# Optimization experiments

Hardware: AMD Instinct MI355X
Metric: run time of the kernel (lower is better)

## Reference

```python
import jax, jax.numpy as jnp
import numpy as np

B, S, D, H = 4, 2048, 256, 8
SPARSITY = 0.1


def setup_inputs() -> dict:
    key = jax.random.key(0)
    ks = jax.random.split(key, 6)
    s = 0.02
    return {
        "x": jax.random.normal(ks[0], (B, S, D), jnp.float32),
        # nn.MultiheadAttention packed in-projection (W_q;W_k;W_v) and out-projection
        "w_in": jax.random.normal(ks[1], (3 * D, D), jnp.float32) * s,
        "b_in": jnp.zeros((3 * D,), jnp.float32),
        "w_out": jax.random.normal(ks[2], (D, D), jnp.float32) * s,
        "b_out": jnp.zeros((D,), jnp.float32),
        # sparsity gate: Linear(D, D//4) -> ReLU -> Linear(D//4, 1) -> Sigmoid
        "gate_w1": jax.random.normal(ks[3], (D // 4, D), jnp.float32) * s,
        "gate_b1": jnp.zeros((D // 4,), jnp.float32),
        "gate_w2": jax.random.normal(ks[4], (1, D // 4), jnp.float32) * s,
        "gate_b2": jnp.zeros((1,), jnp.float32),
    }


def reference(x, w_in, b_in, w_out, b_out, gate_w1, gate_b1, gate_w2, gate_b2):
    b, s, d = x.shape
    hd = d // H

    # --- adaptive sparse mask (top-k importance gating) ---
    h = jax.nn.relu(jnp.einsum('bsd,fd->bsf', x, gate_w1) + gate_b1)
    importance = jax.nn.sigmoid(jnp.einsum('bsf,of->bso', h, gate_w2) + gate_b2)[..., 0]  # [B,S]
    k = max(1, int(s * SPARSITY))
    _, top_idx = jax.lax.top_k(importance, k)  # [B,k]
    keep = jnp.zeros((b, s), dtype=bool).at[jnp.arange(b)[:, None], top_idx].set(True)  # [B,S]

    # --- multi-head attention with key_padding_mask = ~keep ---
    qkv = jnp.einsum('bsd,ed->bse', x, w_in) + b_in  # [B,S,3D]
    q, kk, v = jnp.split(qkv, 3, axis=-1)
    split_heads = lambda t: t.reshape(b, s, H, hd).transpose(0, 2, 1, 3)  # [B,H,S,hd]
    q, kk, v = split_heads(q), split_heads(kk), split_heads(v)

    scores = jnp.einsum('bhqd,bhkd->bhqk', q, kk) / jnp.sqrt(jnp.asarray(hd, x.dtype))
    neg = jnp.finfo(scores.dtype).min
    scores = jnp.where(keep[:, None, None, :], scores, neg)  # mask non-selected keys
    attn = jax.nn.softmax(scores, axis=-1)

    out = jnp.einsum('bhqk,bhkd->bhqd', attn, v)
    out = out.transpose(0, 2, 1, 3).reshape(b, s, d)
    return jnp.einsum('bsd,od->bso', out, w_out) + b_out
```

## Files before the change

### kernel.cpp

```cpp
#include <hip/hip_runtime.h>
#include <hip/hip_bf16.h>

#define B_  4
#define S_  2048
#define D_  256
#define H_  8
#define HD_ 32
#define K_  204
#define SCALE_ 0.17677669529663687f

#define OFF_IMP    0
#define OFF_META   8192
#define OFF_KIDX   8208
#define OFF_KG     9232
#define OFF_VT     113680
#define OFF_Q      228368
#define OFF_XH     1276944
#define OFF_XL     2325520
#define OFF_AOH    3374096
#define OFF_AOL    4422672
#define OFF_WIH    5471248
#define OFF_WIL    5569552
#define OFF_WOH    5667856
#define OFF_WOL    5700624

#define GSTR 80
#define PSTR 228
#define VSTR 232

typedef __attribute__((ext_vector_type(8))) short short8v;
typedef __attribute__((ext_vector_type(4))) float f32x4;

static __device__ __forceinline__ unsigned short f2bf(float f) {
    unsigned int u = __float_as_uint(f);
    u += 0x7FFFu + ((u >> 16) & 1u);
    return (unsigned short)(u >> 16);
}
static __device__ __forceinline__ float bf2f(unsigned short h) {
    return __uint_as_float((unsigned int)h << 16);
}
static __device__ __forceinline__ short8v ld_bf8(const unsigned short* p) {
    union { unsigned int u[4]; short8v v; } cv;
    const uint2 a  = *(const uint2*)(p);
    const uint2 b2 = *(const uint2*)(p + 4);
    cv.u[0] = a.x; cv.u[1] = a.y; cv.u[2] = b2.x; cv.u[3] = b2.y;
    return cv.v;
}
static __device__ __forceinline__ void split_store8(
    const float* __restrict__ src, unsigned short* dh, unsigned short* dl)
{
    short8v h, l;
    #pragma unroll
    for (int e = 0; e < 8; ++e) {
        const float f = src[e];
        const unsigned short hh = f2bf(f);
        h[e] = (short)hh;
        l[e] = (short)f2bf(f - bf2f(hh));
    }
    *(short8v*)dh = h;
    *(short8v*)dl = l;
}

__global__ __launch_bounds__(256) void gate_kernel(
    const float* __restrict__ x, const float* __restrict__ gw1,
    const float* __restrict__ gb1, const float* __restrict__ gw2,
    const float* __restrict__ w_in, const float* __restrict__ w_out, float* ws)
{
    const int t0 = blockIdx.x * 8;
    const int tid = threadIdx.x;
    __shared__ __align__(16) float xs[8 * D_];
    __shared__ float hred[8 * 64];

    const float4* src = (const float4*)(x + (size_t)t0 * D_);
    ((float4*)xs)[tid]       = src[tid];
    ((float4*)xs)[tid + 256] = src[tid + 256];
    __syncthreads();

    {
        unsigned short* XH = (unsigned short*)(ws + OFF_XH);
        unsigned short* XL = (unsigned short*)(ws + OFF_XL);
        split_store8(xs + tid * 8, XH + (size_t)t0 * D_ + tid * 8,
                                   XL + (size_t)t0 * D_ + tid * 8);
    }
    if (blockIdx.x < 128) {
        const int e0 = blockIdx.x * 2048 + tid * 8;
        if (e0 < 196608) {
            split_store8(w_in + e0, (unsigned short*)(ws + OFF_WIH) + e0,
                                    (unsigned short*)(ws + OFF_WIL) + e0);
        } else {
            const int e = e0 - 196608;
            split_store8(w_out + e, (unsigned short*)(ws + OFF_WOH) + e,
                                    (unsigned short*)(ws + OFF_WOL) + e);
        }
    }
    if (blockIdx.x == 0 && tid < 16) ((int*)(ws + OFF_META))[tid] = 0;

    const int c = tid & 3, f = tid >> 2;
    float4 wv[16];
    const float4* wr = (const float4*)(gw1 + (size_t)f * D_) + c;
    #pragma unroll
    for (int j = 0; j < 16; ++j) wv[j] = wr[j * 4];
    const float bb = gb1[f], g2 = gw2[f];

    #pragma unroll
    for (int tk = 0; tk < 8; ++tk) {
        const float4* xr = (const float4*)(xs + tk * D_) + c;
        float a = 0.0f;
        #pragma unroll
        for (int j = 0; j < 16; ++j) {
            float4 xv = xr[j * 4];
            a += wv[j].x*xv.x + wv[j].y*xv.y + wv[j].z*xv.z + wv[j].w*xv.w;
        }
        a += __shfl_xor(a, 1);
        a += __shfl_xor(a, 2);
        if (c == 0) hred[tk * 64 + f] = fmaxf(a + bb, 0.0f) * g2;
    }
    __syncthreads();

    const int tk = tid >> 5, ln = tid & 31;
    float s = hred[tk * 64 + ln] + hred[tk * 64 + ln + 32];
    #pragma unroll
    for (int o = 16; o; o >>= 1) s += __shfl_xor(s, o, 32);
    if (ln == 0) ws[OFF_IMP + t0 + tk] = s;
}

__global__ __launch_bounds__(256) void rank_kernel(
    const float* __restrict__ ws_imp, int* kidx, int* meta)
{
    const int b  = blockIdx.x >> 7;
    const int ic = blockIdx.x & 127;
    const int tid = threadIdx.x;
    __shared__ __align__(16) float vs[S_];
    const float* src = ws_imp + b * S_;
    #pragma unroll
    for (int cc = 0; cc < 2; ++cc)
        ((float4*)vs)[tid + cc*256] = ((const float4*)src)[tid + cc*256];
    __syncthreads();

    const int il = tid >> 4;
    const int c  = tid & 15;
    const int i  = ic * 16 + il;
    const float vi = vs[i];
    int gt = 0, eq = 0;
    const float4* v4 = (const float4*)vs + c * 32;
    #pragma unroll 8
    for (int t = 0; t < 32; ++t) {
        const int j4 = (t + c) & 31;
        float4 w = v4[j4];
        const int base = c * 128 + j4 * 4;
        gt += (w.x > vi); eq += (w.x == vi) && (base + 0 < i);
        gt += (w.y > vi); eq += (w.y == vi) && (base + 1 < i);
        gt += (w.z > vi); eq += (w.z == vi) && (base + 2 < i);
        gt += (w.w > vi); eq += (w.w == vi) && (base + 3 < i);
    }
    int r = gt + eq;
    r += __shfl_xor(r, 1);
    r += __shfl_xor(r, 2);
    r += __shfl_xor(r, 4);
    r += __shfl_xor(r, 8);
    if (c == 0 && r < K_) {
        const int p = atomicAdd(&meta[2 + b], 1);
        kidx[b * K_ + p] = i;
    }
}

__global__ __launch_bounds__(256) void proj_kernel(
    const unsigned short* __restrict__ XH, const unsigned short* __restrict__ XL,
    const unsigned short* __restrict__ WIH, const unsigned short* __restrict__ WIL,
    const float* __restrict__ b_in, unsigned short* __restrict__ Qb,
    unsigned short* __restrict__ KG, unsigned short* __restrict__ VTg,
    const int* __restrict__ kidx)
{
    __shared__ __align__(16) unsigned short Ash[64 * GSTR];
    __shared__ __align__(16) unsigned short Asl[64 * GSTR];
    __shared__ __align__(16) unsigned short Bsh[64 * GSTR];
    __shared__ __align__(16) unsigned short Bsl[64 * GSTR];

    const int tid = threadIdx.x;
    const bool isQ = (blockIdx.x < 128);
    const int lane = tid & 63, w = tid >> 6;
    const int c = lane & 15, g = lane >> 4;
    const int mq = w >> 1, nq = w & 1;
    const int srow = tid >> 2, sseg = tid & 3;

    int m0, n0, b = blockIdx.y;
    size_t arow;
    int brow;
    if (isQ) {
        m0 = blockIdx.x * 64; n0 = blockIdx.y * 64;
        arow = (size_t)(m0 + srow);
        brow = n0 + srow;
    } else {
        const int kx = blockIdx.x - 128;
        m0 = (kx & 3) * 64; n0 = (kx >> 2) * 64;
        const int tok = kidx[b * K_ + min(m0 + srow, K_ - 1)];
        arow = (size_t)b * S_ + tok;
        brow = D_ + n0 + srow;
    }
    const unsigned short* Aph = XH + arow * D_ + sseg * 16;
    const unsigned short* Apl = XL + arow * D_ + sseg * 16;
    const unsigned short* Bph = WIH + (size_t)brow * D_ + sseg * 16;
    const unsigned short* Bpl = WIL + (size_t)brow * D_ + sseg * 16;

    const f32x4 zf = {0.0f, 0.0f, 0.0f, 0.0f};
    f32x4 acc[2][2] = {{zf, zf}, {zf, zf}};

    short8v arh[2], arl[2], brh[2], brl[2];
    #pragma unroll
    for (int u = 0; u < 2; ++u) {
        arh[u] = *(const short8v*)(Aph + u*8); arl[u] = *(const short8v*)(Apl + u*8);
        brh[u] = *(const short8v*)(Bph + u*8); brl[u] = *(const short8v*)(Bpl + u*8);
    }

    for (int k0 = 0; k0 < D_; k0 += 64) {
        __syncthreads();
        #pragma unroll
        for (int u = 0; u < 2; ++u) {
            *(short8v*)&Ash[srow*GSTR + sseg*16 + u*8] = arh[u];
            *(short8v*)&Asl[srow*GSTR + sseg*16 + u*8] = arl[u];
            *(short8v*)&Bsh[srow*GSTR + sseg*16 + u*8] = brh[u];
            *(short8v*)&Bsl[srow*GSTR + sseg*16 + u*8] = brl[u];
        }
        __syncthreads();
        if (k0 + 64 < D_) {
            #pragma unroll
            for (int u = 0; u < 2; ++u) {
                arh[u] = *(const short8v*)(Aph + k0 + 64 + u*8);
                arl[u] = *(const short8v*)(Apl + k0 + 64 + u*8);
                brh[u] = *(const short8v*)(Bph + k0 + 64 + u*8);
                brl[u] = *(const short8v*)(Bpl + k0 + 64 + u*8);
            }
        }
        #pragma unroll
        for (int ks = 0; ks < 2; ++ks) {
            short8v am[2][2], bm[2][2];
            #pragma unroll
            for (int t = 0; t < 2; ++t) {
                const int ra = (mq*32 + t*16 + c) * GSTR + ks*32 + g*8;
                am[t][0] = *(const short8v*)&Ash[ra];
                am[t][1] = *(const short8v*)&Asl[ra];
                const int rb = (nq*32 + t*16 + c) * GSTR + ks*32 + g*8;
                bm[t][0] = *(const short8v*)&Bsh[rb];
                bm[t][1] = *(const short8v*)&Bsl[rb];
            }
            #pragma unroll
            for (int mt = 0; mt < 2; ++mt)
                #pragma unroll
                for (int nt = 0; nt < 2; ++nt) {
                    acc[mt][nt] = __builtin_amdgcn_mfma_f32_16x16x32_bf16(am[mt][0], bm[nt][0], acc[mt][nt], 0, 0, 0);
                    acc[mt][nt] = __builtin_amdgcn_mfma_f32_16x16x32_bf16(am[mt][0], bm[nt][1], acc[mt][nt], 0, 0, 0);
                    acc[mt][nt] = __builtin_amdgcn_mfma_f32_16x16x32_bf16(am[mt][1], bm[nt][0], acc[mt][nt], 0, 0, 0);
                }
        }
    }

    if (isQ) {
        #pragma unroll
        for (int nt = 0; nt < 2; ++nt) {
            const int n = n0 + nq*32 + nt*16 + c;
            const float bv = b_in[n];
            #pragma unroll
            for (int mt = 0; mt < 2; ++mt) {
                const int m = m0 + mq*32 + mt*16 + g*4;
                #pragma unroll
                for (int r = 0; r < 4; ++r)
                    Qb[(size_t)(m + r) * D_ + n] = f2bf(acc[mt][nt][r] + bv);
            }
        }
    } else {
        #pragma unroll
        for (int nt = 0; nt < 2; ++nt) {
            const int n = n0 + nq*32 + nt*16 + c;
            const float bv = b_in[D_ + n];
            #pragma unroll
            for (int mt = 0; mt < 2; ++mt) {
                const int j = m0 + mq*32 + mt*16 + g*4;
                #pragma unroll
                for (int r = 0; r < 4; ++r) {
                    const int jj = j + r;
                    if (n < 256) {
                        if (jj < K_)
                            KG[((size_t)b * K_ + jj) * 256 + n] = f2bf(acc[mt][nt][r] + bv);
                    } else {
                        if (jj < 224)
                            VTg[((size_t)b * 256 + (n - 256)) * 224 + jj] =
                                (jj < K_) ? f2bf(acc[mt][nt][r] + bv) : (unsigned short)0;
                    }
                }
            }
        }
    }
}

__global__ __launch_bounds__(256) void gemm_kernel(
    const unsigned short* __restrict__ Ah, const unsigned short* __restrict__ Al,
    const unsigned short* __restrict__ Bh, const unsigned short* __restrict__ Bl,
    const float* __restrict__ bias, float* __restrict__ Cf)
{
    __shared__ __align__(16) unsigned short Ash[64 * GSTR];
    __shared__ __align__(16) unsigned short Asl[64 * GSTR];
    __shared__ __align__(16) unsigned short Bsh[64 * GSTR];
    __shared__ __align__(16) unsigned short Bsl[64 * GSTR];

    const int tid = threadIdx.x;
    const int m0 = blockIdx.x * 64, n0 = blockIdx.y * 64;
    const int lane = tid & 63, w = tid >> 6;
    const int c = lane & 15, g = lane >> 4;
    const int mq = w >> 1, nq = w & 1;

    const f32x4 zf = {0.0f, 0.0f, 0.0f, 0.0f};
    f32x4 acc[2][2] = {{zf, zf}, {zf, zf}};

    const int srow = tid >> 2, sseg = tid & 3;
    const unsigned short* Aph = Ah + (size_t)(m0 + srow) * D_ + sseg * 16;
    const unsigned short* Apl = Al + (size_t)(m0 + srow) * D_ + sseg * 16;
    const unsigned short* Bph = Bh + (size_t)(n0 + srow) * D_ + sseg * 16;
    const unsigned short* Bpl = Bl + (size_t)(n0 + srow) * D_ + sseg * 16;

    short8v arh[2], arl[2], brh[2], brl[2];
    #pragma unroll
    for (int u = 0; u < 2; ++u) {
        arh[u] = *(const short8v*)(Aph + u*8); arl[u] = *(const short8v*)(Apl + u*8);
        brh[u] = *(const short8v*)(Bph + u*8); brl[u] = *(const short8v*)(Bpl + u*8);
    }

    for (int k0 = 0; k0 < D_; k0 += 64) {
        __syncthreads();
        #pragma unroll
        for (int u = 0; u < 2; ++u) {
            *(short8v*)&Ash[srow*GSTR + sseg*16 + u*8] = arh[u];
            *(short8v*)&Asl[srow*GSTR + sseg*16 + u*8] = arl[u];
            *(short8v*)&Bsh[srow*GSTR + sseg*16 + u*8] = brh[u];
            *(short8v*)&Bsl[srow*GSTR + sseg*16 + u*8] = brl[u];
        }
        __syncthreads();
        if (k0 + 64 < D_) {
            #pragma unroll
            for (int u = 0; u < 2; ++u) {
                arh[u] = *(const short8v*)(Aph + k0 + 64 + u*8);
                arl[u] = *(const short8v*)(Apl + k0 + 64 + u*8);
                brh[u] = *(const short8v*)(Bph + k0 + 64 + u*8);
                brl[u] = *(const short8v*)(Bpl + k0 + 64 + u*8);
            }
        }
        #pragma unroll
        for (int ks = 0; ks < 2; ++ks) {
            short8v am[2][2], bm[2][2];
            #pragma unroll
            for (int t = 0; t < 2; ++t) {
                const int ra = (mq*32 + t*16 + c) * GSTR + ks*32 + g*8;
                am[t][0] = *(const short8v*)&Ash[ra];
                am[t][1] = *(const short8v*)&Asl[ra];
                const int rb = (nq*32 + t*16 + c) * GSTR + ks*32 + g*8;
                bm[t][0] = *(const short8v*)&Bsh[rb];
                bm[t][1] = *(const short8v*)&Bsl[rb];
            }
            #pragma unroll
            for (int mt = 0; mt < 2; ++mt)
                #pragma unroll
                for (int nt = 0; nt < 2; ++nt) {
                    acc[mt][nt] = __builtin_amdgcn_mfma_f32_16x16x32_bf16(am[mt][0], bm[nt][0], acc[mt][nt], 0, 0, 0);
                    acc[mt][nt] = __builtin_amdgcn_mfma_f32_16x16x32_bf16(am[mt][0], bm[nt][1], acc[mt][nt], 0, 0, 0);
                    acc[mt][nt] = __builtin_amdgcn_mfma_f32_16x16x32_bf16(am[mt][1], bm[nt][0], acc[mt][nt], 0, 0, 0);
                }
        }
    }
    #pragma unroll
    for (int nt = 0; nt < 2; ++nt) {
        const int n = n0 + nq*32 + nt*16 + c;
        const float bv = bias[n];
        #pragma unroll
        for (int mt = 0; mt < 2; ++mt) {
            const int m = m0 + mq*32 + mt*16 + g*4;
            #pragma unroll
            for (int r = 0; r < 4; ++r)
                Cf[(size_t)(m + r) * D_ + n] = acc[mt][nt][r] + bv;
        }
    }
}

__global__ __launch_bounds__(256) void attn_kernel(
    const unsigned short* __restrict__ KG, const unsigned short* __restrict__ VTg,
    const unsigned short* __restrict__ Qb,
    unsigned short* __restrict__ aoh, unsigned short* __restrict__ aol)
{
    const int b = blockIdx.z, h = blockIdx.y, q0 = blockIdx.x * 32;
    const int tid = threadIdx.x;
    const int lane = tid & 63, w = tid >> 6;
    const int c = lane & 15, g = lane >> 4;

    __shared__ __align__(16) unsigned short Pl[32 * PSTR];
    __shared__ __align__(16) unsigned short VTl[32 * VSTR];
    __shared__ float redl[4 * 32];
    __shared__ float invl[32];

    const unsigned short* KGb = KG + (size_t)b * K_ * 256;

    {
        const unsigned short* vsrc = VTg + ((size_t)b * 256 + h * HD_) * 224;
        for (int i = tid; i < 32 * 28; i += 256) {
            const int d = i / 28, seg = i % 28;
            *(short8v*)&VTl[d * VSTR + seg * 8] = *(const short8v*)(vsrc + d * 224 + seg * 8);
        }
    }
    {
        const int q = tid >> 3, cc = tid & 7;
        *(unsigned int*)&Pl[q * PSTR + 208 + cc * 2] = 0u;
    }

    short8v qa[2];
    #pragma unroll
    for (int qt = 0; qt < 2; ++qt)
        qa[qt] = *(const short8v*)(Qb + (size_t)(b * S_ + q0 + qt*16 + c) * D_ + h * HD_ + g * 8);

    const int njt = (w == 0) ? 4 : 3;
    f32x4 acc[2][4];
    const f32x4 zf = {0.0f, 0.0f, 0.0f, 0.0f};
    #pragma unroll
    for (int qt = 0; qt < 2; ++qt)
        #pragma unroll
        for (int t = 0; t < 4; ++t) acc[qt][t] = zf;

    for (int t = 0; t < njt; ++t) {
        const int jt = w + 4 * t;
        const int jc = min(jt * 16 + c, K_ - 1);
        const short8v kb = *(const short8v*)(KGb + (size_t)jc * 256 + h * HD_ + g * 8);
        acc[0][t] = __builtin_amdgcn_mfma_f32_16x16x32_bf16(qa[0], kb, acc[0][t], 0, 0, 0);
        acc[1][t] = __builtin_amdgcn_mfma_f32_16x16x32_bf16(qa[1], kb, acc[1][t], 0, 0, 0);
    }

    float rs[2][4] = {{0,0,0,0},{0,0,0,0}};
    for (int t = 0; t < njt; ++t) {
        const int jg = (w + 4 * t) * 16 + c;
        const bool val = (jg < K_);
        #pragma unroll
        for (int qt = 0; qt < 2; ++qt) {
            #pragma unroll
            for (int r = 0; r < 4; ++r) {
                const float e = val ? __expf(acc[qt][t][r] * SCALE_) : 0.0f;
                rs[qt][r] += e;
                Pl[(qt*16 + g*4 + r) * PSTR + jg] = f2bf(e);
            }
        }
    }
    #pragma unroll
    for (int qt = 0; qt < 2; ++qt)
        #pragma unroll
        for (int r = 0; r < 4; ++r) {
            float s = rs[qt][r];
            s += __shfl_xor(s, 1); s += __shfl_xor(s, 2);
            s += __shfl_xor(s, 4); s += __shfl_xor(s, 8);
            if (c == 0) redl[w * 32 + qt*16 + g*4 + r] = s;
        }

    __syncthreads();
    if (tid < 32)
        invl[tid] = 1.0f / (redl[tid] + redl[32 + tid] + redl[64 + tid] + redl[96 + tid]);
    __syncthreads();

    const int dt = w >> 1, qt2 = w & 1;
    f32x4 o = zf;
    const unsigned short* vb = &VTl[(dt*16 + c) * VSTR];
    const unsigned short* pb = &Pl[(qt2*16 + c) * PSTR];
    #pragma unroll
    for (int kt = 0; kt < 7; ++kt) {
        const short8v av = ld_bf8(vb + kt*32 + g*8);
        const short8v bv = ld_bf8(pb + kt*32 + g*8);
        o = __builtin_amdgcn_mfma_f32_16x16x32_bf16(av, bv, o, 0, 0, 0);
    }
    const float iv = invl[qt2*16 + c];
    const size_t oidx = (size_t)(b * S_ + q0 + qt2*16 + c) * D_ + h * HD_ + dt*16 + g*4;
    ushort4 hh, ll;
    {
        const float v0 = o[0]*iv, v1 = o[1]*iv, v2 = o[2]*iv, v3 = o[3]*iv;
        hh.x = f2bf(v0); ll.x = f2bf(v0 - bf2f(hh.x));
        hh.y = f2bf(v1); ll.y = f2bf(v1 - bf2f(hh.y));
        hh.z = f2bf(v2); ll.z = f2bf(v2 - bf2f(hh.z));
        hh.w = f2bf(v3); ll.w = f2bf(v3 - bf2f(hh.w));
    }
    *(ushort4*)(aoh + oidx) = hh;
    *(ushort4*)(aol + oidx) = ll;
}

extern "C" void kernel_launch(void* const* d_in, const int* in_sizes, int n_in,
                              void* d_out, int out_size, void* d_ws, size_t ws_size,
                              hipStream_t stream)
{
    const float* x     = (const float*)d_in[0];
    const float* w_in  = (const float*)d_in[1];
    const float* b_in  = (const float*)d_in[2];
    const float* w_out = (const float*)d_in[3];
    const float* b_out = (const float*)d_in[4];
    const float* gw1   = (const float*)d_in[5];
    const float* gb1   = (const float*)d_in[6];
    const float* gw2   = (const float*)d_in[7];

    float* ws = (float*)d_ws;
    int* meta = (int*)(ws + OFF_META);
    int* kidx = (int*)(ws + OFF_KIDX);
    unsigned short* KG  = (unsigned short*)(ws + OFF_KG);
    unsigned short* VTg = (unsigned short*)(ws + OFF_VT);
    unsigned short* Qb  = (unsigned short*)(ws + OFF_Q);
    unsigned short* XH  = (unsigned short*)(ws + OFF_XH);
    unsigned short* XL  = (unsigned short*)(ws + OFF_XL);
    unsigned short* AOH = (unsigned short*)(ws + OFF_AOH);
    unsigned short* AOL = (unsigned short*)(ws + OFF_AOL);
    unsigned short* WIH = (unsigned short*)(ws + OFF_WIH);
    unsigned short* WIL = (unsigned short*)(ws + OFF_WIL);
    unsigned short* WOH = (unsigned short*)(ws + OFF_WOH);
    unsigned short* WOL = (unsigned short*)(ws + OFF_WOL);
    float* out = (float*)d_out;

    gate_kernel<<<B_ * S_ / 8, 256, 0, stream>>>(x, gw1, gb1, gw2, w_in, w_out, ws);
    rank_kernel<<<B_ * 128, 256, 0, stream>>>(ws + OFF_IMP, kidx, meta);
    proj_kernel<<<dim3(160, 4), 256, 0, stream>>>(
        XH, XL, WIH, WIL, b_in, Qb, KG, VTg, kidx);
    attn_kernel<<<dim3(S_ / 32, H_, B_), 256, 0, stream>>>(KG, VTg, Qb, AOH, AOL);
    gemm_kernel<<<dim3(B_ * S_ / 64, D_ / 64), 256, 0, stream>>>(
        AOH, AOL, WOH, WOL, b_out, out);
}
```

Before: 143.5 us.

## Fuse attention and output projection into one kernel with per-block head loop

Measured after the change: 171.9 us. +19.8%, slower.

```diff
diff --git a/kernel.cpp b/kernel.cpp
--- a/kernel.cpp
+++ b/kernel.cpp
@@ -17,16 +17,15 @@
 #define OFF_Q      228368
 #define OFF_XH     1276944
 #define OFF_XL     2325520
-#define OFF_AOH    3374096
-#define OFF_AOL    4422672
-#define OFF_WIH    5471248
-#define OFF_WIL    5569552
-#define OFF_WOH    5667856
-#define OFF_WOL    5700624
+#define OFF_WIH    3374096
+#define OFF_WIL    3472400
+#define OFF_WOH    3570704
+#define OFF_WOL    3603472
 
 #define GSTR 80
 #define PSTR 228
 #define VSTR 232
+#define AOSTR 264
 
 typedef __attribute__((ext_vector_type(8))) short short8v;
 typedef __attribute__((ext_vector_type(4))) float f32x4;
@@ -292,194 +291,159 @@
     }
 }
 
-__global__ __launch_bounds__(256) void gemm_kernel(
-    const unsigned short* __restrict__ Ah, const unsigned short* __restrict__ Al,
-    const unsigned short* __restrict__ Bh, const unsigned short* __restrict__ Bl,
-    const float* __restrict__ bias, float* __restrict__ Cf)
-{
-    __shared__ __align__(16) unsigned short Ash[64 * GSTR];
-    __shared__ __align__(16) unsigned short Asl[64 * GSTR];
-    __shared__ __align__(16) unsigned short Bsh[64 * GSTR];
-    __shared__ __align__(16) unsigned short Bsl[64 * GSTR];
-
-    const int tid = threadIdx.x;
-    const int m0 = blockIdx.x * 64, n0 = blockIdx.y * 64;
-    const int lane = tid & 63, w = tid >> 6;
-    const int c = lane & 15, g = lane >> 4;
-    const int mq = w >> 1, nq = w & 1;
-
-    const f32x4 zf = {0.0f, 0.0f, 0.0f, 0.0f};
-    f32x4 acc[2][2] = {{zf, zf}, {zf, zf}};
-
-    const int srow = tid >> 2, sseg = tid & 3;
-    const unsigned short* Aph = Ah + (size_t)(m0 + srow) * D_ + sseg * 16;
-    const unsigned short* Apl = Al + (size_t)(m0 + srow) * D_ + sseg * 16;
-    const unsigned short* Bph = Bh + (size_t)(n0 + srow) * D_ + sseg * 16;
-    const unsigned short* Bpl = Bl + (size_t)(n0 + srow) * D_ + sseg * 16;
-
-    short8v arh[2], arl[2], brh[2], brl[2];
-    #pragma unroll
-    for (int u = 0; u < 2; ++u) {
-        arh[u] = *(const short8v*)(Aph + u*8); arl[u] = *(const short8v*)(Apl + u*8);
-        brh[u] = *(const short8v*)(Bph + u*8); brl[u] = *(const short8v*)(Bpl + u*8);
-    }
-
-    for (int k0 = 0; k0 < D_; k0 += 64) {
-        __syncthreads();
-        #pragma unroll
-        for (int u = 0; u < 2; ++u) {
-            *(short8v*)&Ash[srow*GSTR + sseg*16 + u*8] = arh[u];
-            *(short8v*)&Asl[srow*GSTR + sseg*16 + u*8] = arl[u];
-            *(short8v*)&Bsh[srow*GSTR + sseg*16 + u*8] = brh[u];
-            *(short8v*)&Bsl[srow*GSTR + sseg*16 + u*8] = brl[u];
-        }
-        __syncthreads();
-        if (k0 + 64 < D_) {
-            #pragma unroll
-            for (int u = 0; u < 2; ++u) {
-                arh[u] = *(const short8v*)(Aph + k0 + 64 + u*8);
-                arl[u] = *(const short8v*)(Apl + k0 + 64 + u*8);
-                brh[u] = *(const short8v*)(Bph + k0 + 64 + u*8);
-                brl[u] = *(const short8v*)(Bpl + k0 + 64 + u*8);
-            }
-        }
-        #pragma unroll
-        for (int ks = 0; ks < 2; ++ks) {
-            short8v am[2][2], bm[2][2];
-            #pragma unroll
-            for (int t = 0; t < 2; ++t) {
-                const int ra = (mq*32 + t*16 + c) * GSTR + ks*32 + g*8;
-                am[t][0] = *(const short8v*)&Ash[ra];
-                am[t][1] = *(const short8v*)&Asl[ra];
-                const int rb = (nq*32 + t*16 + c) * GSTR + ks*32 + g*8;
-                bm[t][0] = *(const short8v*)&Bsh[rb];
-                bm[t][1] = *(const short8v*)&Bsl[rb];
-            }
-            #pragma unroll
-            for (int mt = 0; mt < 2; ++mt)
-                #pragma unroll
-                for (int nt = 0; nt < 2; ++nt) {
-                    acc[mt][nt] = __builtin_amdgcn_mfma_f32_16x16x32_bf16(am[mt][0], bm[nt][0], acc[mt][nt], 0, 0, 0);
-                    acc[mt][nt] = __builtin_amdgcn_mfma_f32_16x16x32_bf16(am[mt][0], bm[nt][1], acc[mt][nt], 0, 0, 0);
-                    acc[mt][nt] = __builtin_amdgcn_mfma_f32_16x16x32_bf16(am[mt][1], bm[nt][0], acc[mt][nt], 0, 0, 0);
-                }
-        }
-    }
-    #pragma unroll
-    for (int nt = 0; nt < 2; ++nt) {
-        const int n = n0 + nq*32 + nt*16 + c;
-        const float bv = bias[n];
-        #pragma unroll
-        for (int mt = 0; mt < 2; ++mt) {
-            const int m = m0 + mq*32 + mt*16 + g*4;
-            #pragma unroll
-            for (int r = 0; r < 4; ++r)
-                Cf[(size_t)(m + r) * D_ + n] = acc[mt][nt][r] + bv;
-        }
-    }
-}
-
-__global__ __launch_bounds__(256) void attn_kernel(
+__global__ __launch_bounds__(256) void fused_attn_kernel(
     const unsigned short* __restrict__ KG, const unsigned short* __restrict__ VTg,
     const unsigned short* __restrict__ Qb,
-    unsigned short* __restrict__ aoh, unsigned short* __restrict__ aol)
-{
-    const int b = blockIdx.z, h = blockIdx.y, q0 = blockIdx.x * 32;
+    const unsigned short* __restrict__ WOH, const unsigned short* __restrict__ WOL,
+    const float* __restrict__ b_out, float* __restrict__ out)
+{
+    const int bb = blockIdx.y, q0 = blockIdx.x * 32;
     const int tid = threadIdx.x;
     const int lane = tid & 63, w = tid >> 6;
     const int c = lane & 15, g = lane >> 4;
 
     __shared__ __align__(16) unsigned short Pl[32 * PSTR];
     __shared__ __align__(16) unsigned short VTl[32 * VSTR];
+    __shared__ __align__(16) unsigned short AOHl[32 * AOSTR];
+    __shared__ __align__(16) unsigned short AOLl[32 * AOSTR];
     __shared__ float redl[4 * 32];
     __shared__ float invl[32];
 
-    const unsigned short* KGb = KG + (size_t)b * K_ * 256;
-
-    {
-        const unsigned short* vsrc = VTg + ((size_t)b * 256 + h * HD_) * 224;
-        for (int i = tid; i < 32 * 28; i += 256) {
-            const int d = i / 28, seg = i % 28;
-            *(short8v*)&VTl[d * VSTR + seg * 8] = *(const short8v*)(vsrc + d * 224 + seg * 8);
-        }
-    }
+    const unsigned short* KGb = KG + (size_t)bb * K_ * 256;
+    const f32x4 zf = {0.0f, 0.0f, 0.0f, 0.0f};
+
     {
         const int q = tid >> 3, cc = tid & 7;
         *(unsigned int*)&Pl[q * PSTR + 208 + cc * 2] = 0u;
     }
 
-    short8v qa[2];
-    #pragma unroll
-    for (int qt = 0; qt < 2; ++qt)
-        qa[qt] = *(const short8v*)(Qb + (size_t)(b * S_ + q0 + qt*16 + c) * D_ + h * HD_ + g * 8);
-
-    const int njt = (w == 0) ? 4 : 3;
-    f32x4 acc[2][4];
-    const f32x4 zf = {0.0f, 0.0f, 0.0f, 0.0f};
-    #pragma unroll
-    for (int qt = 0; qt < 2; ++qt)
-        #pragma unroll
-        for (int t = 0; t < 4; ++t) acc[qt][t] = zf;
-
-    for (int t = 0; t < njt; ++t) {
-        const int jt = w + 4 * t;
-        const int jc = min(jt * 16 + c, K_ - 1);
-        const short8v kb = *(const short8v*)(KGb + (size_t)jc * 256 + h * HD_ + g * 8);
-        acc[0][t] = __builtin_amdgcn_mfma_f32_16x16x32_bf16(qa[0], kb, acc[0][t], 0, 0, 0);
-        acc[1][t] = __builtin_amdgcn_mfma_f32_16x16x32_bf16(qa[1], kb, acc[1][t], 0, 0, 0);
-    }
-
-    float rs[2][4] = {{0,0,0,0},{0,0,0,0}};
-    for (int t = 0; t < njt; ++t) {
-        const int jg = (w + 4 * t) * 16 + c;
-        const bool val = (jg < K_);
-        #pragma unroll
-        for (int qt = 0; qt < 2; ++qt) {
+    for (int h = 0; h < H_; ++h) {
+        {
+            const unsigned short* vsrc = VTg + ((size_t)bb * 256 + h * HD_) * 224;
+            for (int i = tid; i < 32 * 28; i += 256) {
+                const int d = i / 28, seg = i % 28;
+                *(short8v*)&VTl[d * VSTR + seg * 8] = *(const short8v*)(vsrc + d * 224 + seg * 8);
+            }
+        }
+
+        short8v qa[2];
+        #pragma unroll
+        for (int qt = 0; qt < 2; ++qt)
+            qa[qt] = *(const short8v*)(Qb + (size_t)(bb * S_ + q0 + qt*16 + c) * D_ + h * HD_ + g * 8);
+
+        const int njt = (w == 0) ? 4 : 3;
+        f32x4 acc[2][4];
+        #pragma unroll
+        for (int qt = 0; qt < 2; ++qt)
+            #pragma unroll
+            for (int t = 0; t < 4; ++t) acc[qt][t] = zf;
+
+        for (int t = 0; t < njt; ++t) {
+            const int jt = w + 4 * t;
+            const int jc = min(jt * 16 + c, K_ - 1);
+            const short8v kb = *(const short8v*)(KGb + (size_t)jc * 256 + h * HD_ + g * 8);
+            acc[0][t] = __builtin_amdgcn_mfma_f32_16x16x32_bf16(qa[0], kb, acc[0][t], 0, 0, 0);
+            acc[1][t] = __builtin_amdgcn_mfma_f32_16x16x32_bf16(qa[1], kb, acc[1][t], 0, 0, 0);
+        }
+
+        float rs[2][4] = {{0,0,0,0},{0,0,0,0}};
+        for (int t = 0; t < njt; ++t) {
+            const int jg = (w + 4 * t) * 16 + c;
+            const bool val = (jg < K_);
+            #pragma unroll
+            for (int qt = 0; qt < 2; ++qt) {
+                #pragma unroll
+                for (int r = 0; r < 4; ++r) {
+                    const float e = val ? __expf(acc[qt][t][r] * SCALE_) : 0.0f;
+                    rs[qt][r] += e;
+                    Pl[(qt*16 + g*4 + r) * PSTR + jg] = f2bf(e);
+                }
+            }
+        }
+        #pragma unroll
+        for (int qt = 0; qt < 2; ++qt)
             #pragma unroll
             for (int r = 0; r < 4; ++r) {
-                const float e = val ? __expf(acc[qt][t][r] * SCALE_) : 0.0f;
-                rs[qt][r] += e;
-                Pl[(qt*16 + g*4 + r) * PSTR + jg] = f2bf(e);
-            }
-        }
-    }
-    #pragma unroll
-    for (int qt = 0; qt < 2; ++qt)
-        #pragma unroll
-        for (int r = 0; r < 4; ++r) {
-            float s = rs[qt][r];
-            s += __shfl_xor(s, 1); s += __shfl_xor(s, 2);
-            s += __shfl_xor(s, 4); s += __shfl_xor(s, 8);
-            if (c == 0) redl[w * 32 + qt*16 + g*4 + r] = s;
-        }
-
-    __syncthreads();
-    if (tid < 32)
-        invl[tid] = 1.0f / (redl[tid] + redl[32 + tid] + redl[64 + tid] + redl[96 + tid]);
-    __syncthreads();
-
-    const int dt = w >> 1, qt2 = w & 1;
-    f32x4 o = zf;
-    const unsigned short* vb = &VTl[(dt*16 + c) * VSTR];
-    const unsigned short* pb = &Pl[(qt2*16 + c) * PSTR];
-    #pragma unroll
-    for (int kt = 0; kt < 7; ++kt) {
-        const short8v av = ld_bf8(vb + kt*32 + g*8);
-        const short8v bv = ld_bf8(pb + kt*32 + g*8);
-        o = __builtin_amdgcn_mfma_f32_16x16x32_bf16(av, bv, o, 0, 0, 0);
-    }
-    const float iv = invl[qt2*16 + c];
-    const size_t oidx = (size_t)(b * S_ + q0 + qt2*16 + c) * D_ + h * HD_ + dt*16 + g*4;
-    ushort4 hh, ll;
+                float s = rs[qt][r];
+                s += __shfl_xor(s, 1); s += __shfl_xor(s, 2);
+                s += __shfl_xor(s, 4); s += __shfl_xor(s, 8);
+                if (c == 0) redl[w * 32 + qt*16 + g*4 + r] = s;
+            }
+
+        __syncthreads();
+        if (tid < 32)
+            invl[tid] = 1.0f / (redl[tid] + redl[32 + tid] + redl[64 + tid] + redl[96 + tid]);
+        __syncthreads();
+
+        const int dt = w >> 1, qt2 = w & 1;
+        f32x4 o = zf;
+        const unsigned short* vb = &VTl[(dt*16 + c) * VSTR];
+        const unsigned short* pb = &Pl[(qt2*16 + c) * PSTR];
+        #pragma unroll
+        for (int kt = 0; kt < 7; ++kt) {
+            const short8v av = ld_bf8(vb + kt*32 + g*8);
+            const short8v bv = ld_bf8(pb + kt*32 + g*8);
+            o = __builtin_amdgcn_mfma_f32_16x16x32_bf16(av, bv, o, 0, 0, 0);
+        }
+        const float iv = invl[qt2*16 + c];
+        const int aoff = (qt2*16 + c) * AOSTR + h * HD_ + dt*16 + g*4;
+        ushort4 hh, ll;
+        {
+            const float v0 = o[0]*iv, v1 = o[1]*iv, v2 = o[2]*iv, v3 = o[3]*iv;
+            hh.x = f2bf(v0); ll.x = f2bf(v0 - bf2f(hh.x));
+            hh.y = f2bf(v1); ll.y = f2bf(v1 - bf2f(hh.y));
+            hh.z = f2bf(v2); ll.z = f2bf(v2 - bf2f(hh.z));
+            hh.w = f2bf(v3); ll.w = f2bf(v3 - bf2f(hh.w));
+        }
+        *(ushort4*)&AOHl[aoff] = hh;
+        *(ushort4*)&AOLl[aoff] = ll;
+
+        __syncthreads();
+    }
+
     {
-        const float v0 = o[0]*iv, v1 = o[1]*iv, v2 = o[2]*iv, v3 = o[3]*iv;
-        hh.x = f2bf(v0); ll.x = f2bf(v0 - bf2f(hh.x));
-        hh.y = f2bf(v1); ll.y = f2bf(v1 - bf2f(hh.y));
-        hh.z = f2bf(v2); ll.z = f2bf(v2 - bf2f(hh.z));
-        hh.w = f2bf(v3); ll.w = f2bf(v3 - bf2f(hh.w));
-    }
-    *(ushort4*)(aoh + oidx) = hh;
-    *(ushort4*)(aol + oidx) = ll;
+        const int nbase = w * 64;
+        f32x4 acc2[2][4];
+        #pragma unroll
+        for (int mt = 0; mt < 2; ++mt)
+            #pragma unroll
+            for (int nt = 0; nt < 4; ++nt) acc2[mt][nt] = zf;
+
+        #pragma unroll 2
+        for (int ks = 0; ks < 8; ++ks) {
+            short8v ah[2], al[2];
+            #pragma unroll
+            for (int mt = 0; mt < 2; ++mt) {
+                const int ro = (mt*16 + c) * AOSTR + ks*32 + g*8;
+                ah[mt] = *(const short8v*)&AOHl[ro];
+                al[mt] = *(const short8v*)&AOLl[ro];
+            }
+            #pragma unroll
+            for (int nt = 0; nt < 4; ++nt) {
+                const size_t wr = (size_t)(nbase + nt*16 + c) * D_ + ks*32 + g*8;
+                const short8v bh = *(const short8v*)(WOH + wr);
+                const short8v bl = *(const short8v*)(WOL + wr);
+                #pragma unroll
+                for (int mt = 0; mt < 2; ++mt) {
+                    acc2[mt][nt] = __builtin_amdgcn_mfma_f32_16x16x32_bf16(ah[mt], bh, acc2[mt][nt], 0, 0, 0);
+                    acc2[mt][nt] = __builtin_amdgcn_mfma_f32_16x16x32_bf16(ah[mt], bl, acc2[mt][nt], 0, 0, 0);
+                    acc2[mt][nt] = __builtin_amdgcn_mfma_f32_16x16x32_bf16(al[mt], bh, acc2[mt][nt], 0, 0, 0);
+                }
+            }
+        }
+        #pragma unroll
+        for (int nt = 0; nt < 4; ++nt) {
+            const int n = nbase + nt*16 + c;
+            const float bv = b_out[n];
+            #pragma unroll
+            for (int mt = 0; mt < 2; ++mt) {
+                const int m = mt*16 + g*4;
+                #pragma unroll
+                for (int r = 0; r < 4; ++r)
+                    out[(size_t)(bb * S_ + q0 + m + r) * D_ + n] = acc2[mt][nt][r] + bv;
+            }
+        }
+    }
 }
 
 extern "C" void kernel_launch(void* const* d_in, const int* in_sizes, int n_in,
@@ -503,8 +467,6 @@
     unsigned short* Qb  = (unsigned short*)(ws + OFF_Q);
     unsigned short* XH  = (unsigned short*)(ws + OFF_XH);
     unsigned short* XL  = (unsigned short*)(ws + OFF_XL);
-    unsigned short* AOH = (unsigned short*)(ws + OFF_AOH);
-    unsigned short* AOL = (unsigned short*)(ws + OFF_AOL);
     unsigned short* WIH = (unsigned short*)(ws + OFF_WIH);
     unsigned short* WIL = (unsigned short*)(ws + OFF_WIL);
     unsigned short* WOH = (unsigned short*)(ws + OFF_WOH);
@@ -515,7 +477,6 @@
     rank_kernel<<<B_ * 128, 256, 0, stream>>>(ws + OFF_IMP, kidx, meta);
     proj_kernel<<<dim3(160, 4), 256, 0, stream>>>(
         XH, XL, WIH, WIL, b_in, Qb, KG, VTg, kidx);
-    attn_kernel<<<dim3(S_ / 32, H_, B_), 256, 0, stream>>>(KG, VTg, Qb, AOH, AOL);
-    gemm_kernel<<<dim3(B_ * S_ / 64, D_ / 64), 256, 0, stream>>>(
-        AOH, AOL, WOH, WOL, b_out, out);
-}
+    fused_attn_kernel<<<dim3(S_ / 32, B_), 256, 0, stream>>>(
+        KG, VTg, Qb, WOH, WOL, b_out, out);
+}
```
